# Optimization experiments

Measured on AMD Instinct MI355X. Metric: run time of the kernel, lower is better.

The kernel has to match this reference:

```python
import math
import jax, jax.numpy as jnp
import numpy as np

EMBED_DIM = 1024
NUM_HEADS = 16
HEAD_DIM = EMBED_DIM // NUM_HEADS
ROTARY_DIM = HEAD_DIM  # default: rotary_dim = head_dim
BASE = 10000.0


def _rope_cos_sin(seq_len, d, dtype=jnp.float32):
    # theta: [d/2], positions: [S]
    theta = 1.0 / (BASE ** (jnp.arange(0, d, 2, dtype=jnp.float32) / d))
    pos = jnp.arange(seq_len, dtype=jnp.float32)
    idx_theta = pos[:, None] * theta[None, :]          # [S, d/2]
    idx_theta2 = jnp.concatenate([idx_theta, idx_theta], axis=-1)  # [S, d]
    return jnp.cos(idx_theta2).astype(dtype), jnp.sin(idx_theta2).astype(dtype)


def _apply_rope(x):
    # x: [B, H, S, head_dim]; rotate first ROTARY_DIM features
    S = x.shape[-2]
    cos, sin = _rope_cos_sin(S, ROTARY_DIM, x.dtype)   # [S, ROTARY_DIM]
    x_rope, x_pass = x[..., :ROTARY_DIM], x[..., ROTARY_DIM:]
    d2 = ROTARY_DIM // 2
    neg_half = jnp.concatenate([-x_rope[..., d2:], x_rope[..., :d2]], axis=-1)
    x_rope = x_rope * cos + neg_half * sin
    return jnp.concatenate([x_rope, x_pass], axis=-1)


def setup_inputs() -> dict:
    key = jax.random.key(0)
    ks = jax.random.split(key, 9)
    B, S, E = 4, 2048, EMBED_DIM
    scale = 1.0 / math.sqrt(E)
    inp = {
        "x": jax.random.normal(ks[0], (B, S, E), dtype=jnp.float32),
        "attn_mask": jnp.ones((B, S), dtype=jnp.int32),
        "Wq": jax.random.normal(ks[1], (E, E), dtype=jnp.float32) * scale,
        "bq": jnp.zeros((E,), dtype=jnp.float32),
        "Wk": jax.random.normal(ks[2], (E, E), dtype=jnp.float32) * scale,
        "bk": jnp.zeros((E,), dtype=jnp.float32),
        "Wv": jax.random.normal(ks[3], (E, E), dtype=jnp.float32) * scale,
        "bv": jnp.zeros((E,), dtype=jnp.float32),
        "Wo": jax.random.normal(ks[4], (E, E), dtype=jnp.float32) * scale,
        "bo": jnp.zeros((E,), dtype=jnp.float32),
    }
    return inp


def reference(x, attn_mask, Wq, bq, Wk, bk, Wv, bv, Wo, bo):
    B, S, E = x.shape
    H, D = NUM_HEADS, HEAD_DIM

    def proj(W, b):
        # [B,S,E] -> [B,H,S,D]
        y = jnp.einsum('bse,ef->bsf', x, W) + b
        return y.reshape(B, S, H, D).transpose(0, 2, 1, 3)

    q = _apply_rope(proj(Wq, bq))
    k = _apply_rope(proj(Wk, bk))
    v = proj(Wv, bv)

    scores = jnp.einsum('bhsd,bhtd->bhst', q, k) / math.sqrt(D)  # [B,H,S,S]
    mask = attn_mask[:, None, None, :]  # [B,1,1,S]
    scores = jnp.where(mask == 0, jnp.float32(-1e9).astype(scores.dtype), scores)
    attn = jax.nn.softmax(scores, axis=-1)
    out = jnp.einsum('bhst,bhtd->bhsd', attn, v)  # [B,H,S,D]
    out = out.transpose(0, 2, 1, 3).reshape(B, S, E)
    return jnp.einsum('bse,ef->bsf', out, Wo) + bo
```

## Files before the change

kernel.cpp:

```cpp
#include <hip/hip_runtime.h>
#include <math.h>

typedef __attribute__((ext_vector_type(8))) short short8;
typedef __attribute__((ext_vector_type(4))) float f32x4;
typedef __attribute__((ext_vector_type(4))) unsigned short us4;
typedef __attribute__((ext_vector_type(4))) unsigned int u32x4;
typedef __attribute__((ext_vector_type(4))) int i32x4;
typedef unsigned short u16;
typedef unsigned int u32;

#define LOG2E 1.4426950408889634f

static __device__ __forceinline__ u16 f2bf(float f){
  u32 u = __builtin_bit_cast(u32, f);
  u = (u + 0x7FFFu + ((u >> 16) & 1u)) >> 16;
  return (u16)u;
}

static __device__ __forceinline__ void gload16(const void* g, void* l){
  __builtin_amdgcn_global_load_lds((const __attribute__((address_space(1))) void*)g,
                                   (__attribute__((address_space(3))) void*)l,
                                   16, 0, 0);
}

static __device__ __forceinline__ f32x4 mfma16(short8 a, short8 b, f32x4 c){
  return __builtin_amdgcn_mfma_f32_16x16x32_bf16(a, b, c, 0, 0, 0);
}

__global__ void rope_tab_k(float* __restrict__ cosT, float* __restrict__ sinT){
  int idx = blockIdx.x * 256 + threadIdx.x;
  int s = idx >> 5, i = idx & 31;
  double th = pow(10000.0, -((double)(2 * i)) / 64.0);
  float ang = (float)s * (float)th;
  cosT[idx] = (float)cos((double)ang);
  sinT[idx] = (float)sin((double)ang);
}

__global__ void cvt_x_k(const float* __restrict__ x, u16* __restrict__ xb, int n){
  int i = (blockIdx.x * 256 + threadIdx.x) * 4;
  if (i >= n) return;
  f32x4 v = *(const f32x4*)(x + i);
  us4 o; o[0]=f2bf(v[0]); o[1]=f2bf(v[1]); o[2]=f2bf(v[2]); o[3]=f2bf(v[3]);
  *(us4*)(xb + i) = o;
}

__global__ void wt_cvt_k(const float* __restrict__ W0, const float* __restrict__ W1,
                         const float* __restrict__ W2, const float* __restrict__ W3,
                         u16* __restrict__ out){
  __shared__ float t[32][33];
  const float* W = (blockIdx.z == 0) ? W0 : (blockIdx.z == 1) ? W1 : (blockIdx.z == 2) ? W2 : W3;
  u16* O = out + (size_t)blockIdx.z * 1024 * 1024;
  int tx = threadIdx.x, ty = threadIdx.y;
  int kb = blockIdx.y * 32, nb = blockIdx.x * 32;
  #pragma unroll
  for (int i = 0; i < 4; i++)
    t[ty + i*8][tx] = W[(size_t)(kb + ty + i*8) * 1024 + nb + tx];
  __syncthreads();
  #pragma unroll
  for (int i = 0; i < 4; i++)
    O[(size_t)(nb + ty + i*8) * 1024 + kb + tx] = f2bf(t[tx][ty + i*8]);
}

__global__ __launch_bounds__(256, 2)
void qkv_gemm_k(const u16* __restrict__ A, const u16* __restrict__ WT,
                const float* __restrict__ bq, const float* __restrict__ bk,
                const float* __restrict__ bv,
                const float* __restrict__ cosT, const float* __restrict__ sinT,
                u16* __restrict__ Qr, u16* __restrict__ Kr, u16* __restrict__ Vt)
{
  __shared__ __align__(16) u16 Al[128][64];
  __shared__ __align__(16) u16 Bl[128][64];
  const int mode = blockIdx.y >> 3;
  const int cy   = blockIdx.y & 7;
  const u16* BT = WT + (size_t)mode * 1024 * 1024;
  const float* bias = (mode == 0) ? bq : (mode == 1) ? bk : bv;
  u16* outB = (mode == 0) ? Qr : (mode == 1) ? Kr : Vt;

  const int tid = threadIdx.x;
  const int w = tid >> 6, lane = tid & 63, g = lane >> 4, c = lane & 15;
  const int wr = w >> 1, wc = w & 1;
  const int R0 = blockIdx.x * 128, C0 = cy * 128;

  f32x4 acc[4][4];
  const f32x4 vz = {0.f, 0.f, 0.f, 0.f};
  #pragma unroll
  for (int mi = 0; mi < 4; mi++)
    #pragma unroll
    for (int ni = 0; ni < 4; ni++) acc[mi][ni] = vz;

  const u16* gA[4]; const u16* gB[4]; u16* lA[4]; u16* lB[4];
  #pragma unroll
  for (int i = 0; i < 4; i++){
    int I = w * 4 + i;
    int rr = I * 8 + (lane >> 3), kk = (lane & 7) * 8;
    gA[i] = A  + (size_t)(R0 + rr) * 1024 + kk;
    gB[i] = BT + (size_t)(C0 + rr) * 1024 + kk;
    lA[i] = &Al[I * 8][0];
    lB[i] = &Bl[I * 8][0];
  }

  for (int t = 0; t < 16; ++t){
    const int k0 = t * 64;
    #pragma unroll
    for (int i = 0; i < 4; i++){
      gload16(gA[i] + k0, lA[i]);
      gload16(gB[i] + k0, lB[i]);
    }
    __syncthreads();
    #pragma unroll
    for (int ki = 0; ki < 2; ++ki){
      short8 af[4], bfr[4];
      #pragma unroll
      for (int mi = 0; mi < 4; mi++) af[mi]  = *(const short8*)&Al[wr*64 + mi*16 + c][ki*32 + g*8];
      #pragma unroll
      for (int ni = 0; ni < 4; ni++) bfr[ni] = *(const short8*)&Bl[wc*64 + ni*16 + c][ki*32 + g*8];
      #pragma unroll
      for (int mi = 0; mi < 4; mi++)
        #pragma unroll
        for (int ni = 0; ni < 4; ni++)
          acc[mi][ni] = mfma16(af[mi], bfr[ni], acc[mi][ni]);
    }
    __syncthreads();
  }

  if (mode == 2){
    int h = cy * 2 + wc;
    #pragma unroll
    for (int ni = 0; ni < 4; ni++){
      int col = C0 + wc*64 + ni*16 + c;
      int d = ni*16 + c;
      float bvv = bias[col];
      #pragma unroll
      for (int mi = 0; mi < 4; mi++){
        int row0 = R0 + wr*64 + mi*16 + g*4;
        int b = row0 >> 11, s0 = row0 & 2047;
        us4 pk;
        #pragma unroll
        for (int r = 0; r < 4; r++) pk[r] = f2bf(acc[mi][ni][r] + bvv);
        *(us4*)&outB[((size_t)(b*16 + h)*64 + d)*2048 + s0] = pk;
      }
    }
  } else {
    int h = cy * 2 + wc;
    const float qs = (mode == 0) ? 0.125f : 1.0f;
    float bvv[4];
    #pragma unroll
    for (int ni = 0; ni < 4; ni++) bvv[ni] = bias[C0 + wc*64 + ni*16 + c];
    #pragma unroll
    for (int mi = 0; mi < 4; mi++){
      int row0 = R0 + wr*64 + mi*16 + g*4;
      int b = row0 >> 11;
      #pragma unroll
      for (int r = 0; r < 4; r++){
        int s = (row0 + r) & 2047;
        float v0 = acc[mi][0][r] + bvv[0];
        float v1 = acc[mi][1][r] + bvv[1];
        float v2 = acc[mi][2][r] + bvv[2];
        float v3 = acc[mi][3][r] + bvv[3];
        float ca = cosT[s*32 + c],      sa = sinT[s*32 + c];
        float cb = cosT[s*32 + 16 + c], sb = sinT[s*32 + 16 + c];
        float o0 = (v0*ca - v2*sa) * qs, o2 = (v2*ca + v0*sa) * qs;
        float o1 = (v1*cb - v3*sb) * qs, o3 = (v3*cb + v1*sb) * qs;
        size_t base = ((size_t)(b*16 + h)*2048 + s)*64;
        outB[base +  0 + c] = f2bf(o0);
        outB[base + 16 + c] = f2bf(o1);
        outB[base + 32 + c] = f2bf(o2);
        outB[base + 48 + c] = f2bf(o3);
      }
    }
  }
}

__global__ __launch_bounds__(256, 2)
void out_gemm_k(const u16* __restrict__ A, const u16* __restrict__ BT,
                const float* __restrict__ bias, float* __restrict__ outF)
{
  __shared__ __align__(16) u16 Al[128][64];
  __shared__ __align__(16) u16 Bl[128][64];
  const int tid = threadIdx.x;
  const int w = tid >> 6, lane = tid & 63, g = lane >> 4, c = lane & 15;
  const int wr = w >> 1, wc = w & 1;
  const int R0 = blockIdx.x * 128, C0 = blockIdx.y * 128;

  f32x4 acc[4][4];
  const f32x4 vz = {0.f, 0.f, 0.f, 0.f};
  #pragma unroll
  for (int mi = 0; mi < 4; mi++)
    #pragma unroll
    for (int ni = 0; ni < 4; ni++) acc[mi][ni] = vz;

  const u16* gA[4]; const u16* gB[4]; u16* lA[4]; u16* lB[4];
  #pragma unroll
  for (int i = 0; i < 4; i++){
    int I = w * 4 + i;
    int rr = I * 8 + (lane >> 3), kk = (lane & 7) * 8;
    gA[i] = A  + (size_t)(R0 + rr) * 1024 + kk;
    gB[i] = BT + (size_t)(C0 + rr) * 1024 + kk;
    lA[i] = &Al[I * 8][0];
    lB[i] = &Bl[I * 8][0];
  }

  for (int t = 0; t < 16; ++t){
    const int k0 = t * 64;
    #pragma unroll
    for (int i = 0; i < 4; i++){
      gload16(gA[i] + k0, lA[i]);
      gload16(gB[i] + k0, lB[i]);
    }
    __syncthreads();
    #pragma unroll
    for (int ki = 0; ki < 2; ++ki){
      short8 af[4], bfr[4];
      #pragma unroll
      for (int mi = 0; mi < 4; mi++) af[mi]  = *(const short8*)&Al[wr*64 + mi*16 + c][ki*32 + g*8];
      #pragma unroll
      for (int ni = 0; ni < 4; ni++) bfr[ni] = *(const short8*)&Bl[wc*64 + ni*16 + c][ki*32 + g*8];
      #pragma unroll
      for (int mi = 0; mi < 4; mi++)
        #pragma unroll
        for (int ni = 0; ni < 4; ni++)
          acc[mi][ni] = mfma16(af[mi], bfr[ni], acc[mi][ni]);
    }
    __syncthreads();
  }

  #pragma unroll
  for (int mi = 0; mi < 4; mi++){
    #pragma unroll
    for (int ni = 0; ni < 4; ni++){
      int col = C0 + wc*64 + ni*16 + c;
      float bvv = bias[col];
      int row0 = R0 + wr*64 + mi*16 + g*4;
      #pragma unroll
      for (int r = 0; r < 4; r++)
        outF[(size_t)(row0 + r) * 1024 + col] = acc[mi][ni][r] + bvv;
    }
  }
}

__global__ __launch_bounds__(256, 4)
void attn_fwd_k(const u16* __restrict__ Q, const u16* __restrict__ K, const u16* __restrict__ V,
                const int* __restrict__ msk, u16* __restrict__ AO)
{
  __shared__ __align__(16) u16 Kl[2][64][64];
  __shared__ __align__(16) u16 Vl[2][64][64];
  __shared__ __align__(8) unsigned char Ml[2048];
  const int tid = threadIdx.x;
  const int w = tid >> 6, lane = tid & 63, g = lane >> 4, c = lane & 15;

  const int lin = blockIdx.y * 16 + blockIdx.x;
  const int v_  = (lin & 7) * 128 + (lin >> 3);
  const int bh = v_ >> 4, b = bh >> 4, h = bh & 15;
  const int qw = (v_ & 15) * 128 + w * 32;

  {
    const int* mp = msk + b*2048 + tid*8;
    i32x4 a = *(const i32x4*)mp;
    i32x4 d2 = *(const i32x4*)(mp + 4);
    u32 lo = (a[0]  ? 1u : 0u) | (a[1]  ? 0x100u : 0u) | (a[2]  ? 0x10000u : 0u) | (a[3]  ? 0x1000000u : 0u);
    u32 hi = (d2[0] ? 1u : 0u) | (d2[1] ? 0x100u : 0u) | (d2[2] ? 0x10000u : 0u) | (d2[3] ? 0x1000000u : 0u);
    *(u32*)&Ml[tid*8]     = lo;
    *(u32*)&Ml[tid*8 + 4] = hi;
  }
  asm volatile("s_waitcnt lgkmcnt(0)" ::: "memory");

  short8 qb[2][2];
  #pragma unroll
  for (int mq = 0; mq < 2; mq++)
    #pragma unroll
    for (int ki = 0; ki < 2; ki++)
      qb[mq][ki] = *(const short8*)&Q[((size_t)bh*2048 + qw + mq*16 + c)*64 + ki*32 + g*8];

  const int l3 = lane >> 3, l7 = lane & 7;
  const int scol = (l7 ^ l3) * 8;
  const u16* gK[2]; const u16* gV[2];
  #pragma unroll
  for (int i = 0; i < 2; i++){
    int s = (w*2 + i)*8 + l3;
    int ps = (s & 0x20) | ((s & 0x10) >> 2) | ((s & 0x0C) << 1) | (s & 3);
    gK[i] = K + ((size_t)bh*2048 + ps)*64 + scol;
    gV[i] = V + ((size_t)bh*64 + s)*2048 + scol;
  }
  #pragma unroll
  for (int i = 0; i < 2; i++){
    gload16(gK[i], &Kl[0][(w*2+i)*8][0]);
    gload16(gV[i], &Vl[0][(w*2+i)*8][0]);
  }

  f32x4 oacc[2][4];
  float mrun[2], lrun[2];
  const f32x4 vz = {0.f, 0.f, 0.f, 0.f};
  #pragma unroll
  for (int mq = 0; mq < 2; mq++){
    #pragma unroll
    for (int nd = 0; nd < 4; nd++) oacc[mq][nd] = vz;
    mrun[mq] = -1e30f; lrun[mq] = 0.f;
  }

  const int cs0 = (g*8) ^ ((c & 7) << 3);
  const int cs1 = (32 + g*8) ^ ((c & 7) << 3);

  for (int t = 0; t < 32; ++t){
    {
      const size_t ko = (size_t)(t+1) * 64 * 64;
      const size_t vo = (size_t)(t+1) * 64;
      #pragma unroll
      for (int i = 0; i < 2; i++){
        gload16(gK[i] + ko, &Kl[(t+1)&1][(w*2+i)*8][0]);
        gload16(gV[i] + vo, &Vl[(t+1)&1][(w*2+i)*8][0]);
      }
    }
    asm volatile("s_waitcnt vmcnt(4)" ::: "memory");
    __builtin_amdgcn_s_barrier();
    asm volatile("" ::: "memory");

    const u16* Kb = &Kl[t&1][0][0];
    const u16* Vb = &Vl[t&1][0][0];
    const int t0 = t * 64;

    f32x4 sacc[4][2];
    #pragma unroll
    for (int nt = 0; nt < 4; nt++){ sacc[nt][0] = vz; sacc[nt][1] = vz; }
    #pragma unroll
    for (int ki = 0; ki < 2; ki++){
      const int cs = ki ? cs1 : cs0;
      short8 ka[4];
      #pragma unroll
      for (int nt = 0; nt < 4; nt++) ka[nt] = *(const short8*)&Kb[(nt*16 + c)*64 + cs];
      #pragma unroll
      for (int nt = 0; nt < 4; nt++)
        #pragma unroll
        for (int mq = 0; mq < 2; mq++)
          sacc[nt][mq] = mfma16(ka[nt], qb[mq][ki], sacc[nt][mq]);
    }

    {
      const u32 mw0 = *(const u32*)&Ml[t0 + 8*g];
      const u32 mw1 = *(const u32*)&Ml[t0 + 8*g + 4];
      const u32 mw2 = *(const u32*)&Ml[t0 + 32 + 8*g];
      const u32 mw3 = *(const u32*)&Ml[t0 + 32 + 8*g + 4];
      if (!__all((mw0 & mw1 & mw2 & mw3) == 0x01010101u)){
        const u32 mw[4] = {mw0, mw1, mw2, mw3};
        #pragma unroll
        for (int nt = 0; nt < 4; nt++)
          #pragma unroll
          for (int r = 0; r < 4; r++)
            if (((mw[nt] >> (8*r)) & 0xFFu) == 0){ sacc[nt][0][r] = -1e9f; sacc[nt][1][r] = -1e9f; }
      }
    }

    float pm[2];
    #pragma unroll
    for (int mq = 0; mq < 2; mq++){
      float a0 = fmaxf(fmaxf(sacc[0][mq][0], sacc[0][mq][1]), fmaxf(sacc[0][mq][2], sacc[0][mq][3]));
      float a1 = fmaxf(fmaxf(sacc[1][mq][0], sacc[1][mq][1]), fmaxf(sacc[1][mq][2], sacc[1][mq][3]));
      float a2 = fmaxf(fmaxf(sacc[2][mq][0], sacc[2][mq][1]), fmaxf(sacc[2][mq][2], sacc[2][mq][3]));
      float a3 = fmaxf(fmaxf(sacc[3][mq][0], sacc[3][mq][1]), fmaxf(sacc[3][mq][2], sacc[3][mq][3]));
      float mm = fmaxf(fmaxf(a0, a1), fmaxf(a2, a3));
      mm = fmaxf(mm, __shfl_xor(mm, 16, 64));
      mm = fmaxf(mm, __shfl_xor(mm, 32, 64));
      pm[mq] = mm;
    }

    if (__any((pm[0] > mrun[0] + 8.f) | (pm[1] > mrun[1] + 8.f))){
      float al[2];
      #pragma unroll
      for (int mq = 0; mq < 2; mq++){
        float mn = fmaxf(mrun[mq], pm[mq]);
        al[mq] = exp2f((mrun[mq] - mn) * LOG2E);
        mrun[mq] = mn;
        lrun[mq] *= al[mq];
      }
      #pragma unroll
      for (int mq = 0; mq < 2; mq++){
        float b0 = __shfl(al[mq], g*4 + 0, 64);
        float b1 = __shfl(al[mq], g*4 + 1, 64);
        float b2 = __shfl(al[mq], g*4 + 2, 64);
        float b3 = __shfl(al[mq], g*4 + 3, 64);
        #pragma unroll
        for (int nd = 0; nd < 4; nd++){
          oacc[mq][nd][0] *= b0; oacc[mq][nd][1] *= b1;
          oacc[mq][nd][2] *= b2; oacc[mq][nd][3] *= b3;
        }
      }
    }

    short8 pa[2][2];
    #pragma unroll
    for (int mq = 0; mq < 2; mq++){
      const float nm = -mrun[mq] * LOG2E;
      float p[16]; u32 rb[16];
      #pragma unroll
      for (int nt = 0; nt < 4; nt++)
        #pragma unroll
        for (int r = 0; r < 4; r++){
          float pp = exp2f(fmaf(sacc[nt][mq][r], LOG2E, nm));
          p[nt*4 + r] = pp;
          u32 u = __builtin_bit_cast(u32, pp);
          rb[nt*4 + r] = u + 0x7FFFu + ((u >> 16) & 1u);
        }
      float s0 = (p[0] + p[1]) + (p[2] + p[3]);
      float s1 = (p[4] + p[5]) + (p[6] + p[7]);
      float s2 = (p[8] + p[9]) + (p[10] + p[11]);
      float s3 = (p[12] + p[13]) + (p[14] + p[15]);
      float sum = (s0 + s1) + (s2 + s3);
      sum += __shfl_xor(sum, 16, 64);
      sum += __shfl_xor(sum, 32, 64);
      lrun[mq] += sum;
      u32x4 q0 = { __builtin_amdgcn_perm(rb[1],  rb[0],  0x07060302u),
                   __builtin_amdgcn_perm(rb[3],  rb[2],  0x07060302u),
                   __builtin_amdgcn_perm(rb[5],  rb[4],  0x07060302u),
                   __builtin_amdgcn_perm(rb[7],  rb[6],  0x07060302u) };
      u32x4 q1 = { __builtin_amdgcn_perm(rb[9],  rb[8],  0x07060302u),
                   __builtin_amdgcn_perm(rb[11], rb[10], 0x07060302u),
                   __builtin_amdgcn_perm(rb[13], rb[12], 0x07060302u),
                   __builtin_amdgcn_perm(rb[15], rb[14], 0x07060302u) };
      pa[mq][0] = __builtin_bit_cast(short8, q0);
      pa[mq][1] = __builtin_bit_cast(short8, q1);
    }

    #pragma unroll
    for (int ki = 0; ki < 2; ki++){
      const int cs = ki ? cs1 : cs0;
      short8 va[4];
      #pragma unroll
      for (int nd = 0; nd < 4; nd++) va[nd] = *(const short8*)&Vb[(nd*16 + c)*64 + cs];
      #pragma unroll
      for (int mq = 0; mq < 2; mq++)
        #pragma unroll
        for (int nd = 0; nd < 4; nd++)
          oacc[mq][nd] = mfma16(pa[mq][ki], va[nd], oacc[mq][nd]);
    }

    asm volatile("" ::: "memory");
    __builtin_amdgcn_s_barrier();
    asm volatile("" ::: "memory");
  }

  #pragma unroll
  for (int mq = 0; mq < 2; mq++){
    #pragma unroll
    for (int r = 0; r < 4; r++){
      float li = __shfl(lrun[mq], g*4 + r, 64);
      float inv = 1.0f / li;
      int q = qw + mq*16 + g*4 + r;
      size_t base = ((size_t)b*2048 + q)*1024 + h*64;
      #pragma unroll
      for (int nd = 0; nd < 4; nd++)
        AO[base + nd*16 + c] = f2bf(oacc[mq][nd][r] * inv);
    }
  }
}

extern "C" void kernel_launch(void* const* d_in, const int* in_sizes, int n_in,
                              void* d_out, int out_size, void* d_ws, size_t ws_size,
                              hipStream_t stream)
{
  const float* x  = (const float*)d_in[0];
  const int* mask = (const int*)d_in[1];
  const float* Wq = (const float*)d_in[2];
  const float* bq = (const float*)d_in[3];
  const float* Wk = (const float*)d_in[4];
  const float* bk = (const float*)d_in[5];
  const float* Wv = (const float*)d_in[6];
  const float* bv = (const float*)d_in[7];
  const float* Wo = (const float*)d_in[8];
  const float* bo = (const float*)d_in[9];
  float* out = (float*)d_out;
  (void)in_sizes; (void)n_in; (void)out_size; (void)ws_size;

  char* ws = (char*)d_ws;
  size_t off = 0;
  auto alloc = [&](size_t bytes){ void* p = ws + off; off += (bytes + 255) & ~(size_t)255; return p; };
  u16* xb    = (u16*)alloc((size_t)8192 * 1024 * 2);
  u16* WT    = (u16*)alloc((size_t)4 * 1024 * 1024 * 2);
  float* cosT = (float*)alloc((size_t)2048 * 32 * 4);
  float* sinT = (float*)alloc((size_t)2048 * 32 * 4);
  u16* Qr    = (u16*)alloc((size_t)8192 * 1024 * 2);
  u16* Kr    = (u16*)alloc((size_t)8192 * 1024 * 2);
  u16* Vt    = (u16*)alloc((size_t)8192 * 1024 * 2);
  u16* AO    = (u16*)alloc((size_t)8192 * 1024 * 2);

  rope_tab_k<<<dim3(256), dim3(256), 0, stream>>>(cosT, sinT);
  cvt_x_k<<<dim3(8192), dim3(256), 0, stream>>>(x, xb, 8192 * 1024);
  wt_cvt_k<<<dim3(32, 32, 4), dim3(32, 8), 0, stream>>>(Wq, Wk, Wv, Wo, WT);

  qkv_gemm_k<<<dim3(64, 24), dim3(256), 0, stream>>>(xb, WT, bq, bk, bv, cosT, sinT, Qr, Kr, Vt);

  attn_fwd_k<<<dim3(16, 64), dim3(256), 0, stream>>>(Qr, Kr, Vt, mask, AO);

  out_gemm_k<<<dim3(64, 8), dim3(256), 0, stream>>>(AO, WT + 3*1024*1024, bo, out);
}
```

Before: 262.7 us.

## Software-pipeline QK^T one tile ahead of softmax and PV in attention

Restructures the flash-attention loop so the QK^T MFMAs for tile t+1 are issued before the softmax and PV of tile t, ping-ponging two score accumulators and prefetching K two tiles ahead. The aim is to overlap matrix-core work with the exp and reduction work and hide LDS latency. It also adds s_setprio around MFMA groups and lowers the occupancy hint from 4 to 3 waves to make room for the extra accumulator registers. The cost is more register pressure and lower occupancy, and the prefetch indexing at the tail loads past K for the last tiles.

```diff
diff --git a/kernel.cpp b/kernel.cpp
--- a/kernel.cpp
+++ b/kernel.cpp
@@ -238,7 +238,7 @@
   }
 }
 
-__global__ __launch_bounds__(256, 4)
+__global__ __launch_bounds__(256, 3)
 void attn_fwd_k(const u16* __restrict__ Q, const u16* __restrict__ K, const u16* __restrict__ V,
                 const int* __restrict__ msk, u16* __restrict__ AO)
 {
@@ -253,6 +253,30 @@
   const int bh = v_ >> 4, b = bh >> 4, h = bh & 15;
   const int qw = (v_ & 15) * 128 + w * 32;
 
+  short8 qb[2][2];
+  #pragma unroll
+  for (int mq = 0; mq < 2; mq++)
+    #pragma unroll
+    for (int ki = 0; ki < 2; ki++)
+      qb[mq][ki] = *(const short8*)&Q[((size_t)bh*2048 + qw + mq*16 + c)*64 + ki*32 + g*8];
+
+  const int l3 = lane >> 3, l7 = lane & 7;
+  const int scol = (l7 ^ l3) * 8;
+  const u16* gK[2]; const u16* gV[2];
+  #pragma unroll
+  for (int i = 0; i < 2; i++){
+    int s = (w*2 + i)*8 + l3;
+    int ps = (s & 0x20) | ((s & 0x10) >> 2) | ((s & 0x0C) << 1) | (s & 3);
+    gK[i] = K + ((size_t)bh*2048 + ps)*64 + scol;
+    gV[i] = V + ((size_t)bh*64 + s)*2048 + scol;
+  }
+  #pragma unroll
+  for (int i = 0; i < 2; i++) gload16(gK[i], &Kl[0][(w*2+i)*8][0]);
+  #pragma unroll
+  for (int i = 0; i < 2; i++) gload16(gV[i], &Vl[0][(w*2+i)*8][0]);
+  #pragma unroll
+  for (int i = 0; i < 2; i++) gload16(gK[i] + (size_t)64*64, &Kl[1][(w*2+i)*8][0]);
+
   {
     const int* mp = msk + b*2048 + tid*8;
     i32x4 a = *(const i32x4*)mp;
@@ -264,29 +288,6 @@
   }
   asm volatile("s_waitcnt lgkmcnt(0)" ::: "memory");
 
-  short8 qb[2][2];
-  #pragma unroll
-  for (int mq = 0; mq < 2; mq++)
-    #pragma unroll
-    for (int ki = 0; ki < 2; ki++)
-      qb[mq][ki] = *(const short8*)&Q[((size_t)bh*2048 + qw + mq*16 + c)*64 + ki*32 + g*8];
-
-  const int l3 = lane >> 3, l7 = lane & 7;
-  const int scol = (l7 ^ l3) * 8;
-  const u16* gK[2]; const u16* gV[2];
-  #pragma unroll
-  for (int i = 0; i < 2; i++){
-    int s = (w*2 + i)*8 + l3;
-    int ps = (s & 0x20) | ((s & 0x10) >> 2) | ((s & 0x0C) << 1) | (s & 3);
-    gK[i] = K + ((size_t)bh*2048 + ps)*64 + scol;
-    gV[i] = V + ((size_t)bh*64 + s)*2048 + scol;
-  }
-  #pragma unroll
-  for (int i = 0; i < 2; i++){
-    gload16(gK[i], &Kl[0][(w*2+i)*8][0]);
-    gload16(gV[i], &Vl[0][(w*2+i)*8][0]);
-  }
-
   f32x4 oacc[2][4];
   float mrun[2], lrun[2];
   const f32x4 vz = {0.f, 0.f, 0.f, 0.f};
@@ -300,27 +301,15 @@
   const int cs0 = (g*8) ^ ((c & 7) << 3);
   const int cs1 = (32 + g*8) ^ ((c & 7) << 3);
 
-  for (int t = 0; t < 32; ++t){
-    {
-      const size_t ko = (size_t)(t+1) * 64 * 64;
-      const size_t vo = (size_t)(t+1) * 64;
-      #pragma unroll
-      for (int i = 0; i < 2; i++){
-        gload16(gK[i] + ko, &Kl[(t+1)&1][(w*2+i)*8][0]);
-        gload16(gV[i] + vo, &Vl[(t+1)&1][(w*2+i)*8][0]);
-      }
-    }
-    asm volatile("s_waitcnt vmcnt(4)" ::: "memory");
-    __builtin_amdgcn_s_barrier();
-    asm volatile("" ::: "memory");
-
-    const u16* Kb = &Kl[t&1][0][0];
-    const u16* Vb = &Vl[t&1][0][0];
-    const int t0 = t * 64;
-
-    f32x4 sacc[4][2];
-    #pragma unroll
-    for (int nt = 0; nt < 4; nt++){ sacc[nt][0] = vz; sacc[nt][1] = vz; }
+  f32x4 saccA[4][2], saccB[4][2];
+
+  asm volatile("s_waitcnt vmcnt(4)" ::: "memory");
+  __builtin_amdgcn_s_barrier();
+  asm volatile("" ::: "memory");
+  {
+    #pragma unroll
+    for (int nt = 0; nt < 4; nt++){ saccA[nt][0] = vz; saccA[nt][1] = vz; }
+    const u16* Kb = &Kl[0][0][0];
     #pragma unroll
     for (int ki = 0; ki < 2; ki++){
       const int cs = ki ? cs1 : cs0;
@@ -331,111 +320,158 @@
       for (int nt = 0; nt < 4; nt++)
         #pragma unroll
         for (int mq = 0; mq < 2; mq++)
-          sacc[nt][mq] = mfma16(ka[nt], qb[mq][ki], sacc[nt][mq]);
-    }
-
-    {
-      const u32 mw0 = *(const u32*)&Ml[t0 + 8*g];
-      const u32 mw1 = *(const u32*)&Ml[t0 + 8*g + 4];
-      const u32 mw2 = *(const u32*)&Ml[t0 + 32 + 8*g];
-      const u32 mw3 = *(const u32*)&Ml[t0 + 32 + 8*g + 4];
-      if (!__all((mw0 & mw1 & mw2 & mw3) == 0x01010101u)){
-        const u32 mw[4] = {mw0, mw1, mw2, mw3};
-        #pragma unroll
-        for (int nt = 0; nt < 4; nt++)
-          #pragma unroll
-          for (int r = 0; r < 4; r++)
-            if (((mw[nt] >> (8*r)) & 0xFFu) == 0){ sacc[nt][0][r] = -1e9f; sacc[nt][1][r] = -1e9f; }
-      }
-    }
-
-    float pm[2];
-    #pragma unroll
-    for (int mq = 0; mq < 2; mq++){
-      float a0 = fmaxf(fmaxf(sacc[0][mq][0], sacc[0][mq][1]), fmaxf(sacc[0][mq][2], sacc[0][mq][3]));
-      float a1 = fmaxf(fmaxf(sacc[1][mq][0], sacc[1][mq][1]), fmaxf(sacc[1][mq][2], sacc[1][mq][3]));
-      float a2 = fmaxf(fmaxf(sacc[2][mq][0], sacc[2][mq][1]), fmaxf(sacc[2][mq][2], sacc[2][mq][3]));
-      float a3 = fmaxf(fmaxf(sacc[3][mq][0], sacc[3][mq][1]), fmaxf(sacc[3][mq][2], sacc[3][mq][3]));
-      float mm = fmaxf(fmaxf(a0, a1), fmaxf(a2, a3));
-      mm = fmaxf(mm, __shfl_xor(mm, 16, 64));
-      mm = fmaxf(mm, __shfl_xor(mm, 32, 64));
-      pm[mq] = mm;
-    }
-
-    if (__any((pm[0] > mrun[0] + 8.f) | (pm[1] > mrun[1] + 8.f))){
-      float al[2];
-      #pragma unroll
-      for (int mq = 0; mq < 2; mq++){
-        float mn = fmaxf(mrun[mq], pm[mq]);
-        al[mq] = exp2f((mrun[mq] - mn) * LOG2E);
-        mrun[mq] = mn;
-        lrun[mq] *= al[mq];
-      }
-      #pragma unroll
-      for (int mq = 0; mq < 2; mq++){
-        float b0 = __shfl(al[mq], g*4 + 0, 64);
-        float b1 = __shfl(al[mq], g*4 + 1, 64);
-        float b2 = __shfl(al[mq], g*4 + 2, 64);
-        float b3 = __shfl(al[mq], g*4 + 3, 64);
-        #pragma unroll
-        for (int nd = 0; nd < 4; nd++){
-          oacc[mq][nd][0] *= b0; oacc[mq][nd][1] *= b1;
-          oacc[mq][nd][2] *= b2; oacc[mq][nd][3] *= b3;
-        }
-      }
-    }
-
-    short8 pa[2][2];
-    #pragma unroll
-    for (int mq = 0; mq < 2; mq++){
-      const float nm = -mrun[mq] * LOG2E;
-      float p[16]; u32 rb[16];
-      #pragma unroll
-      for (int nt = 0; nt < 4; nt++)
-        #pragma unroll
-        for (int r = 0; r < 4; r++){
-          float pp = exp2f(fmaf(sacc[nt][mq][r], LOG2E, nm));
-          p[nt*4 + r] = pp;
-          u32 u = __builtin_bit_cast(u32, pp);
-          rb[nt*4 + r] = u + 0x7FFFu + ((u >> 16) & 1u);
-        }
-      float s0 = (p[0] + p[1]) + (p[2] + p[3]);
-      float s1 = (p[4] + p[5]) + (p[6] + p[7]);
-      float s2 = (p[8] + p[9]) + (p[10] + p[11]);
-      float s3 = (p[12] + p[13]) + (p[14] + p[15]);
-      float sum = (s0 + s1) + (s2 + s3);
-      sum += __shfl_xor(sum, 16, 64);
-      sum += __shfl_xor(sum, 32, 64);
-      lrun[mq] += sum;
-      u32x4 q0 = { __builtin_amdgcn_perm(rb[1],  rb[0],  0x07060302u),
-                   __builtin_amdgcn_perm(rb[3],  rb[2],  0x07060302u),
-                   __builtin_amdgcn_perm(rb[5],  rb[4],  0x07060302u),
-                   __builtin_amdgcn_perm(rb[7],  rb[6],  0x07060302u) };
-      u32x4 q1 = { __builtin_amdgcn_perm(rb[9],  rb[8],  0x07060302u),
-                   __builtin_amdgcn_perm(rb[11], rb[10], 0x07060302u),
-                   __builtin_amdgcn_perm(rb[13], rb[12], 0x07060302u),
-                   __builtin_amdgcn_perm(rb[15], rb[14], 0x07060302u) };
-      pa[mq][0] = __builtin_bit_cast(short8, q0);
-      pa[mq][1] = __builtin_bit_cast(short8, q1);
-    }
-
-    #pragma unroll
-    for (int ki = 0; ki < 2; ki++){
-      const int cs = ki ? cs1 : cs0;
-      short8 va[4];
-      #pragma unroll
-      for (int nd = 0; nd < 4; nd++) va[nd] = *(const short8*)&Vb[(nd*16 + c)*64 + cs];
-      #pragma unroll
-      for (int mq = 0; mq < 2; mq++)
-        #pragma unroll
-        for (int nd = 0; nd < 4; nd++)
-          oacc[mq][nd] = mfma16(pa[mq][ki], va[nd], oacc[mq][nd]);
-    }
-
-    asm volatile("" ::: "memory");
-    __builtin_amdgcn_s_barrier();
-    asm volatile("" ::: "memory");
-  }
+          saccA[nt][mq] = mfma16(ka[nt], qb[mq][ki], saccA[nt][mq]);
+    }
+  }
+  asm volatile("" ::: "memory");
+  __builtin_amdgcn_s_barrier();
+  asm volatile("" ::: "memory");
+
+#define SUBITER(TT, SC, SN)                                                          \
+  do {                                                                               \
+    const int tt = (TT);                                                             \
+    const bool last = (tt == 31);                                                    \
+    { const size_t ko = (size_t)(tt+2) * 64 * 64;                                    \
+      const size_t vo = (size_t)(tt+1) * 64;                                         \
+      gload16(gK[0] + ko, &Kl[tt&1][(w*2+0)*8][0]);                                  \
+      gload16(gK[1] + ko, &Kl[tt&1][(w*2+1)*8][0]);                                  \
+      gload16(gV[0] + vo, &Vl[(tt+1)&1][(w*2+0)*8][0]);                              \
+      gload16(gV[1] + vo, &Vl[(tt+1)&1][(w*2+1)*8][0]); }                            \
+    asm volatile("s_waitcnt vmcnt(4)" ::: "memory");                                 \
+    __builtin_amdgcn_s_barrier();                                                    \
+    asm volatile("" ::: "memory");                                                   \
+                           \
+    if (!last){                                                                      \
+      _Pragma("unroll")                                                              \
+      for (int nt = 0; nt < 4; nt++){ SN[nt][0] = vz; SN[nt][1] = vz; }              \
+      const u16* Kb = &Kl[(tt+1)&1][0][0];                                           \
+      _Pragma("unroll")                                                              \
+      for (int ki = 0; ki < 2; ki++){                                                \
+        const int cs = ki ? cs1 : cs0;                                               \
+        short8 ka[4];                                                                \
+        _Pragma("unroll")                                                            \
+        for (int nt = 0; nt < 4; nt++) ka[nt] = *(const short8*)&Kb[(nt*16 + c)*64 + cs]; \
+        __builtin_amdgcn_s_setprio(1);                                               \
+        _Pragma("unroll")                                                            \
+        for (int nt = 0; nt < 4; nt++)                                               \
+          _Pragma("unroll")                                                          \
+          for (int mq = 0; mq < 2; mq++)                                             \
+            SN[nt][mq] = mfma16(ka[nt], qb[mq][ki], SN[nt][mq]);                     \
+        __builtin_amdgcn_s_setprio(0);                                               \
+      }                                                                              \
+    }                                                                                \
+    const u16* Vb = &Vl[tt&1][0][0];                                                 \
+    const int t0 = tt * 64;                                                          \
+                                                                \
+    {                                                                                \
+      const u32 mw0 = *(const u32*)&Ml[t0 + 8*g];                                    \
+      const u32 mw1 = *(const u32*)&Ml[t0 + 8*g + 4];                                \
+      const u32 mw2 = *(const u32*)&Ml[t0 + 32 + 8*g];                               \
+      const u32 mw3 = *(const u32*)&Ml[t0 + 32 + 8*g + 4];                           \
+      if (!__all((mw0 & mw1 & mw2 & mw3) == 0x01010101u)){                           \
+        const u32 mw[4] = {mw0, mw1, mw2, mw3};                                      \
+        _Pragma("unroll")                                                            \
+        for (int nt = 0; nt < 4; nt++)                                               \
+          _Pragma("unroll")                                                          \
+          for (int r = 0; r < 4; r++)                                                \
+            if (((mw[nt] >> (8*r)) & 0xFFu) == 0){ SC[nt][0][r] = -1e9f; SC[nt][1][r] = -1e9f; } \
+      }                                                                              \
+    }                                                                                \
+                                                                \
+    float pm[2];                                                                     \
+    _Pragma("unroll")                                                                \
+    for (int mq = 0; mq < 2; mq++){                                                  \
+      float a0 = fmaxf(fmaxf(SC[0][mq][0], SC[0][mq][1]), fmaxf(SC[0][mq][2], SC[0][mq][3])); \
+      float a1 = fmaxf(fmaxf(SC[1][mq][0], SC[1][mq][1]), fmaxf(SC[1][mq][2], SC[1][mq][3])); \
+      float a2 = fmaxf(fmaxf(SC[2][mq][0], SC[2][mq][1]), fmaxf(SC[2][mq][2], SC[2][mq][3])); \
+      float a3 = fmaxf(fmaxf(SC[3][mq][0], SC[3][mq][1]), fmaxf(SC[3][mq][2], SC[3][mq][3])); \
+      float mm = fmaxf(fmaxf(a0, a1), fmaxf(a2, a3));                                \
+      mm = fmaxf(mm, __shfl_xor(mm, 16, 64));                                        \
+      mm = fmaxf(mm, __shfl_xor(mm, 32, 64));                                        \
+      pm[mq] = mm;                                                                   \
+    }                                                                                \
+                                                              \
+    if (__any((pm[0] > mrun[0] + 8.f) | (pm[1] > mrun[1] + 8.f))){                   \
+      float al[2];                                                                   \
+      _Pragma("unroll")                                                              \
+      for (int mq = 0; mq < 2; mq++){                                                \
+        float mn = fmaxf(mrun[mq], pm[mq]);                                          \
+        al[mq] = exp2f((mrun[mq] - mn) * LOG2E);                                     \
+        mrun[mq] = mn;                                                               \
+        lrun[mq] *= al[mq];                                                          \
+      }                                                                              \
+      _Pragma("unroll")                                                              \
+      for (int mq = 0; mq < 2; mq++){                                                \
+        float b0 = __shfl(al[mq], g*4 + 0, 64);                                      \
+        float b1 = __shfl(al[mq], g*4 + 1, 64);                                      \
+        float b2 = __shfl(al[mq], g*4 + 2, 64);                                      \
+        float b3 = __shfl(al[mq], g*4 + 3, 64);                                      \
+        _Pragma("unroll")                                                            \
+        for (int nd = 0; nd < 4; nd++){                                              \
+          oacc[mq][nd][0] *= b0; oacc[mq][nd][1] *= b1;                              \
+          oacc[mq][nd][2] *= b2; oacc[mq][nd][3] *= b3;                              \
+        }                                                                            \
+      }                                                                              \
+    }                                                                                \
+                   \
+    short8 pa[2][2];                                                                 \
+    _Pragma("unroll")                                                                \
+    for (int mq = 0; mq < 2; mq++){                                                  \
+      const float nm = -mrun[mq] * LOG2E;                                            \
+      float p[16]; u32 rb[16];                                                       \
+      _Pragma("unroll")                                                              \
+      for (int nt = 0; nt < 4; nt++)                                                 \
+        _Pragma("unroll")                                                            \
+        for (int r = 0; r < 4; r++){                                                 \
+          float pp = exp2f(fmaf(SC[nt][mq][r], LOG2E, nm));                          \
+          p[nt*4 + r] = pp;                                                          \
+          u32 u = __builtin_bit_cast(u32, pp);                                       \
+          rb[nt*4 + r] = u + 0x7FFFu + ((u >> 16) & 1u);                             \
+        }                                                                            \
+      float s0 = (p[0] + p[1]) + (p[2] + p[3]);                                      \
+      float s1 = (p[4] + p[5]) + (p[6] + p[7]);                                      \
+      float s2 = (p[8] + p[9]) + (p[10] + p[11]);                                    \
+      float s3 = (p[12] + p[13]) + (p[14] + p[15]);                                  \
+      float sum = (s0 + s1) + (s2 + s3);                                             \
+      sum += __shfl_xor(sum, 16, 64);                                                \
+      sum += __shfl_xor(sum, 32, 64);                                                \
+      lrun[mq] += sum;                                                               \
+      u32x4 q0 = { __builtin_amdgcn_perm(rb[1],  rb[0],  0x07060302u),               \
+                   __builtin_amdgcn_perm(rb[3],  rb[2],  0x07060302u),               \
+                   __builtin_amdgcn_perm(rb[5],  rb[4],  0x07060302u),               \
+                   __builtin_amdgcn_perm(rb[7],  rb[6],  0x07060302u) };             \
+      u32x4 q1 = { __builtin_amdgcn_perm(rb[9],  rb[8],  0x07060302u),               \
+                   __builtin_amdgcn_perm(rb[11], rb[10], 0x07060302u),               \
+                   __builtin_amdgcn_perm(rb[13], rb[12], 0x07060302u),               \
+                   __builtin_amdgcn_perm(rb[15], rb[14], 0x07060302u) };             \
+      pa[mq][0] = __builtin_bit_cast(short8, q0);                                    \
+      pa[mq][1] = __builtin_bit_cast(short8, q1);                                    \
+    }                                                                                \
+                                                                     \
+    _Pragma("unroll")                                                                \
+    for (int ki = 0; ki < 2; ki++){                                                  \
+      const int cs = ki ? cs1 : cs0;                                                 \
+      short8 va[4];                                                                  \
+      _Pragma("unroll")                                                              \
+      for (int nd = 0; nd < 4; nd++) va[nd] = *(const short8*)&Vb[(nd*16 + c)*64 + cs]; \
+      __builtin_amdgcn_s_setprio(1);                                                 \
+      _Pragma("unroll")                                                              \
+      for (int mq = 0; mq < 2; mq++)                                                 \
+        _Pragma("unroll")                                                            \
+        for (int nd = 0; nd < 4; nd++)                                               \
+          oacc[mq][nd] = mfma16(pa[mq][ki], va[nd], oacc[mq][nd]);                   \
+      __builtin_amdgcn_s_setprio(0);                                                 \
+    }                                                                                \
+    asm volatile("" ::: "memory");                                                   \
+    __builtin_amdgcn_s_barrier();                                                    \
+    asm volatile("" ::: "memory");                                                   \
+  } while (0)
+
+  for (int t2 = 0; t2 < 32; t2 += 2){
+    SUBITER(t2,     saccA, saccB);
+    SUBITER(t2 + 1, saccB, saccA);
+  }
+#undef SUBITER
 
   #pragma unroll
   for (int mq = 0; mq < 2; mq++){
```

New measurement: 397.2 us. 1.51x slower.

## Split attention workgroup into 8 waves of 16 query rows each

Applied to the files above, without the earlier changes.

The attention kernel now launches 512 threads per block, and each wave handles 16 query rows instead of 32, which halves per-wave registers and accumulators. The K/V tile loads and mask staging are spread across twice as many threads, and the row-sum cross-lane reduction is deferred to the epilogue rather than done every tile. The aim is higher occupancy and latency hiding. In exchange, each wave reuses every K/V LDS read for only one query block instead of two, so LDS traffic per MFMA doubles, and barriers now synchronize more waves.

```diff
diff --git a/kernel.cpp b/kernel.cpp
--- a/kernel.cpp
+++ b/kernel.cpp
@@ -238,7 +238,7 @@
   }
 }
 
-__global__ __launch_bounds__(256, 4)
+__global__ __launch_bounds__(512, 6)
 void attn_fwd_k(const u16* __restrict__ Q, const u16* __restrict__ K, const u16* __restrict__ V,
                 const int* __restrict__ msk, u16* __restrict__ AO)
 {
@@ -251,66 +251,44 @@
   const int lin = blockIdx.y * 16 + blockIdx.x;
   const int v_  = (lin & 7) * 128 + (lin >> 3);
   const int bh = v_ >> 4, b = bh >> 4, h = bh & 15;
-  const int qw = (v_ & 15) * 128 + w * 32;
-
-  {
-    const int* mp = msk + b*2048 + tid*8;
-    i32x4 a = *(const i32x4*)mp;
-    i32x4 d2 = *(const i32x4*)(mp + 4);
-    u32 lo = (a[0]  ? 1u : 0u) | (a[1]  ? 0x100u : 0u) | (a[2]  ? 0x10000u : 0u) | (a[3]  ? 0x1000000u : 0u);
-    u32 hi = (d2[0] ? 1u : 0u) | (d2[1] ? 0x100u : 0u) | (d2[2] ? 0x10000u : 0u) | (d2[3] ? 0x1000000u : 0u);
-    *(u32*)&Ml[tid*8]     = lo;
-    *(u32*)&Ml[tid*8 + 4] = hi;
-  }
-  asm volatile("s_waitcnt lgkmcnt(0)" ::: "memory");
-
-  short8 qb[2][2];
-  #pragma unroll
-  for (int mq = 0; mq < 2; mq++)
-    #pragma unroll
-    for (int ki = 0; ki < 2; ki++)
-      qb[mq][ki] = *(const short8*)&Q[((size_t)bh*2048 + qw + mq*16 + c)*64 + ki*32 + g*8];
+  const int qw = (v_ & 15) * 128 + w * 16;
+
+  short8 qb[2];
+  #pragma unroll
+  for (int ki = 0; ki < 2; ki++)
+    qb[ki] = *(const short8*)&Q[((size_t)bh*2048 + qw + c)*64 + ki*32 + g*8];
 
   const int l3 = lane >> 3, l7 = lane & 7;
   const int scol = (l7 ^ l3) * 8;
-  const u16* gK[2]; const u16* gV[2];
-  #pragma unroll
-  for (int i = 0; i < 2; i++){
-    int s = (w*2 + i)*8 + l3;
-    int ps = (s & 0x20) | ((s & 0x10) >> 2) | ((s & 0x0C) << 1) | (s & 3);
-    gK[i] = K + ((size_t)bh*2048 + ps)*64 + scol;
-    gV[i] = V + ((size_t)bh*64 + s)*2048 + scol;
-  }
-  #pragma unroll
-  for (int i = 0; i < 2; i++){
-    gload16(gK[i], &Kl[0][(w*2+i)*8][0]);
-    gload16(gV[i], &Vl[0][(w*2+i)*8][0]);
-  }
-
-  f32x4 oacc[2][4];
-  float mrun[2], lrun[2];
+  const int s8 = w*8 + l3;
+  const int ps = (s8 & 0x20) | ((s8 & 0x10) >> 2) | ((s8 & 0x0C) << 1) | (s8 & 3);
+  const u16* gK = K + ((size_t)bh*2048 + ps)*64 + scol;
+  const u16* gV = V + ((size_t)bh*64 + s8)*2048 + scol;
+
+  gload16(gK, &Kl[0][w*8][0]);
+  gload16(gV, &Vl[0][w*8][0]);
+
+  {
+    const int* mp = msk + b*2048 + tid*4;
+    i32x4 a = *(const i32x4*)mp;
+    u32 lo = (a[0] ? 1u : 0u) | (a[1] ? 0x100u : 0u) | (a[2] ? 0x10000u : 0u) | (a[3] ? 0x1000000u : 0u);
+    *(u32*)&Ml[tid*4] = lo;
+  }
+  asm volatile("s_waitcnt lgkmcnt(0)" ::: "memory");
+
+  f32x4 oacc[4];
+  float mrun = -1e30f, lrun = 0.f;
   const f32x4 vz = {0.f, 0.f, 0.f, 0.f};
   #pragma unroll
-  for (int mq = 0; mq < 2; mq++){
-    #pragma unroll
-    for (int nd = 0; nd < 4; nd++) oacc[mq][nd] = vz;
-    mrun[mq] = -1e30f; lrun[mq] = 0.f;
-  }
+  for (int nd = 0; nd < 4; nd++) oacc[nd] = vz;
 
   const int cs0 = (g*8) ^ ((c & 7) << 3);
   const int cs1 = (32 + g*8) ^ ((c & 7) << 3);
 
   for (int t = 0; t < 32; ++t){
-    {
-      const size_t ko = (size_t)(t+1) * 64 * 64;
-      const size_t vo = (size_t)(t+1) * 64;
-      #pragma unroll
-      for (int i = 0; i < 2; i++){
-        gload16(gK[i] + ko, &Kl[(t+1)&1][(w*2+i)*8][0]);
-        gload16(gV[i] + vo, &Vl[(t+1)&1][(w*2+i)*8][0]);
-      }
-    }
-    asm volatile("s_waitcnt vmcnt(4)" ::: "memory");
+    gload16(gK + (size_t)(t+1) * 64 * 64, &Kl[(t+1)&1][w*8][0]);
+    gload16(gV + (size_t)(t+1) * 64,      &Vl[(t+1)&1][w*8][0]);
+    asm volatile("s_waitcnt vmcnt(2)" ::: "memory");
     __builtin_amdgcn_s_barrier();
     asm volatile("" ::: "memory");
 
@@ -318,9 +296,9 @@
     const u16* Vb = &Vl[t&1][0][0];
     const int t0 = t * 64;
 
-    f32x4 sacc[4][2];
-    #pragma unroll
-    for (int nt = 0; nt < 4; nt++){ sacc[nt][0] = vz; sacc[nt][1] = vz; }
+    f32x4 sacc[4];
+    #pragma unroll
+    for (int nt = 0; nt < 4; nt++) sacc[nt] = vz;
     #pragma unroll
     for (int ki = 0; ki < 2; ki++){
       const int cs = ki ? cs1 : cs0;
@@ -329,9 +307,7 @@
       for (int nt = 0; nt < 4; nt++) ka[nt] = *(const short8*)&Kb[(nt*16 + c)*64 + cs];
       #pragma unroll
       for (int nt = 0; nt < 4; nt++)
-        #pragma unroll
-        for (int mq = 0; mq < 2; mq++)
-          sacc[nt][mq] = mfma16(ka[nt], qb[mq][ki], sacc[nt][mq]);
+        sacc[nt] = mfma16(ka[nt], qb[ki], sacc[nt]);
     }
 
     {
@@ -345,56 +321,43 @@
         for (int nt = 0; nt < 4; nt++)
           #pragma unroll
           for (int r = 0; r < 4; r++)
-            if (((mw[nt] >> (8*r)) & 0xFFu) == 0){ sacc[nt][0][r] = -1e9f; sacc[nt][1][r] = -1e9f; }
+            if (((mw[nt] >> (8*r)) & 0xFFu) == 0) sacc[nt][r] = -1e9f;
       }
     }
 
-    float pm[2];
-    #pragma unroll
-    for (int mq = 0; mq < 2; mq++){
-      float a0 = fmaxf(fmaxf(sacc[0][mq][0], sacc[0][mq][1]), fmaxf(sacc[0][mq][2], sacc[0][mq][3]));
-      float a1 = fmaxf(fmaxf(sacc[1][mq][0], sacc[1][mq][1]), fmaxf(sacc[1][mq][2], sacc[1][mq][3]));
-      float a2 = fmaxf(fmaxf(sacc[2][mq][0], sacc[2][mq][1]), fmaxf(sacc[2][mq][2], sacc[2][mq][3]));
-      float a3 = fmaxf(fmaxf(sacc[3][mq][0], sacc[3][mq][1]), fmaxf(sacc[3][mq][2], sacc[3][mq][3]));
-      float mm = fmaxf(fmaxf(a0, a1), fmaxf(a2, a3));
-      mm = fmaxf(mm, __shfl_xor(mm, 16, 64));
-      mm = fmaxf(mm, __shfl_xor(mm, 32, 64));
-      pm[mq] = mm;
-    }
-
-    if (__any((pm[0] > mrun[0] + 8.f) | (pm[1] > mrun[1] + 8.f))){
-      float al[2];
-      #pragma unroll
-      for (int mq = 0; mq < 2; mq++){
-        float mn = fmaxf(mrun[mq], pm[mq]);
-        al[mq] = exp2f((mrun[mq] - mn) * LOG2E);
-        mrun[mq] = mn;
-        lrun[mq] *= al[mq];
+    float a0 = fmaxf(fmaxf(sacc[0][0], sacc[0][1]), fmaxf(sacc[0][2], sacc[0][3]));
+    float a1 = fmaxf(fmaxf(sacc[1][0], sacc[1][1]), fmaxf(sacc[1][2], sacc[1][3]));
+    float a2 = fmaxf(fmaxf(sacc[2][0], sacc[2][1]), fmaxf(sacc[2][2], sacc[2][3]));
+    float a3 = fmaxf(fmaxf(sacc[3][0], sacc[3][1]), fmaxf(sacc[3][2], sacc[3][3]));
+    float pm = fmaxf(fmaxf(a0, a1), fmaxf(a2, a3));
+    pm = fmaxf(pm, __shfl_xor(pm, 16, 64));
+    pm = fmaxf(pm, __shfl_xor(pm, 32, 64));
+
+    if (__any(pm > mrun + 8.f)){
+      float mn = fmaxf(mrun, pm);
+      float al = exp2f((mrun - mn) * LOG2E);
+      mrun = mn;
+      lrun *= al;
+      float b0 = __shfl(al, g*4 + 0, 64);
+      float b1 = __shfl(al, g*4 + 1, 64);
+      float b2 = __shfl(al, g*4 + 2, 64);
+      float b3 = __shfl(al, g*4 + 3, 64);
+      #pragma unroll
+      for (int nd = 0; nd < 4; nd++){
+        oacc[nd][0] *= b0; oacc[nd][1] *= b1;
+        oacc[nd][2] *= b2; oacc[nd][3] *= b3;
       }
-      #pragma unroll
-      for (int mq = 0; mq < 2; mq++){
-        float b0 = __shfl(al[mq], g*4 + 0, 64);
-        float b1 = __shfl(al[mq], g*4 + 1, 64);
-        float b2 = __shfl(al[mq], g*4 + 2, 64);
-        float b3 = __shfl(al[mq], g*4 + 3, 64);
-        #pragma unroll
-        for (int nd = 0; nd < 4; nd++){
-          oacc[mq][nd][0] *= b0; oacc[mq][nd][1] *= b1;
-          oacc[mq][nd][2] *= b2; oacc[mq][nd][3] *= b3;
-        }
-      }
-    }
-
-    short8 pa[2][2];
-    #pragma unroll
-    for (int mq = 0; mq < 2; mq++){
-      const float nm = -mrun[mq] * LOG2E;
+    }
+
+    short8 pa[2];
+    {
+      const float nm = -mrun * LOG2E;
       float p[16]; u32 rb[16];
       #pragma unroll
       for (int nt = 0; nt < 4; nt++)
         #pragma unroll
         for (int r = 0; r < 4; r++){
-          float pp = exp2f(fmaf(sacc[nt][mq][r], LOG2E, nm));
+          float pp = exp2f(fmaf(sacc[nt][r], LOG2E, nm));
           p[nt*4 + r] = pp;
           u32 u = __builtin_bit_cast(u32, pp);
           rb[nt*4 + r] = u + 0x7FFFu + ((u >> 16) & 1u);
@@ -403,10 +366,7 @@
       float s1 = (p[4] + p[5]) + (p[6] + p[7]);
       float s2 = (p[8] + p[9]) + (p[10] + p[11]);
       float s3 = (p[12] + p[13]) + (p[14] + p[15]);
-      float sum = (s0 + s1) + (s2 + s3);
-      sum += __shfl_xor(sum, 16, 64);
-      sum += __shfl_xor(sum, 32, 64);
-      lrun[mq] += sum;
+      lrun += (s0 + s1) + (s2 + s3);
       u32x4 q0 = { __builtin_amdgcn_perm(rb[1],  rb[0],  0x07060302u),
                    __builtin_amdgcn_perm(rb[3],  rb[2],  0x07060302u),
                    __builtin_amdgcn_perm(rb[5],  rb[4],  0x07060302u),
@@ -415,8 +375,8 @@
                    __builtin_amdgcn_perm(rb[11], rb[10], 0x07060302u),
                    __builtin_amdgcn_perm(rb[13], rb[12], 0x07060302u),
                    __builtin_amdgcn_perm(rb[15], rb[14], 0x07060302u) };
-      pa[mq][0] = __builtin_bit_cast(short8, q0);
-      pa[mq][1] = __builtin_bit_cast(short8, q1);
+      pa[0] = __builtin_bit_cast(short8, q0);
+      pa[1] = __builtin_bit_cast(short8, q1);
     }
 
     #pragma unroll
@@ -426,10 +386,8 @@
       #pragma unroll
       for (int nd = 0; nd < 4; nd++) va[nd] = *(const short8*)&Vb[(nd*16 + c)*64 + cs];
       #pragma unroll
-      for (int mq = 0; mq < 2; mq++)
-        #pragma unroll
-        for (int nd = 0; nd < 4; nd++)
-          oacc[mq][nd] = mfma16(pa[mq][ki], va[nd], oacc[mq][nd]);
+      for (int nd = 0; nd < 4; nd++)
+        oacc[nd] = mfma16(pa[ki], va[nd], oacc[nd]);
     }
 
     asm volatile("" ::: "memory");
@@ -437,18 +395,17 @@
     asm volatile("" ::: "memory");
   }
 
-  #pragma unroll
-  for (int mq = 0; mq < 2; mq++){
-    #pragma unroll
-    for (int r = 0; r < 4; r++){
-      float li = __shfl(lrun[mq], g*4 + r, 64);
-      float inv = 1.0f / li;
-      int q = qw + mq*16 + g*4 + r;
-      size_t base = ((size_t)b*2048 + q)*1024 + h*64;
-      #pragma unroll
-      for (int nd = 0; nd < 4; nd++)
-        AO[base + nd*16 + c] = f2bf(oacc[mq][nd][r] * inv);
-    }
+  lrun += __shfl_xor(lrun, 16, 64);
+  lrun += __shfl_xor(lrun, 32, 64);
+  #pragma unroll
+  for (int r = 0; r < 4; r++){
+    float li = __shfl(lrun, g*4 + r, 64);
+    float inv = 1.0f / li;
+    int q = qw + g*4 + r;
+    size_t base = ((size_t)b*2048 + q)*1024 + h*64;
+    #pragma unroll
+    for (int nd = 0; nd < 4; nd++)
+      AO[base + nd*16 + c] = f2bf(oacc[nd][r] * inv);
   }
 }
 
@@ -487,7 +444,7 @@
 
   qkv_gemm_k<<<dim3(64, 24), dim3(256), 0, stream>>>(xb, WT, bq, bk, bv, cosT, sinT, Qr, Kr, Vt);
 
-  attn_fwd_k<<<dim3(16, 64), dim3(256), 0, stream>>>(Qr, Kr, Vt, mask, AO);
+  attn_fwd_k<<<dim3(16, 64), dim3(512), 0, stream>>>(Qr, Kr, Vt, mask, AO);
 
   out_gemm_k<<<dim3(64, 8), dim3(256), 0, stream>>>(AO, WT + 3*1024*1024, bo, out);
 }
```

New measurement: 254.3 us. 1.03x faster.
